# Kernel optimization log

Measured on AMD Instinct MI355X. Metric: run time of the kernel, lower is better.

## Reference

```python
import jax, jax.numpy as jnp
import numpy as np

N, E, D, H, G = 50000, 800000, 256, 256, 64
EPS = 1e-5

def setup_inputs() -> dict:
    key = jax.random.key(0)
    ks = jax.random.split(key, 16)
    s_in = float(np.sqrt(2.0 / D))   # He fan_in init
    s_h = float(np.sqrt(2.0 / H))
    inp = {}
    inp['x'] = jax.random.normal(ks[0], (N, D), jnp.float32)
    inp['edge_index'] = jax.random.randint(ks[1], (2, E), 0, N)
    inp['batch'] = jnp.sort(jax.random.randint(ks[2], (N,), 0, G))
    inp['bn_in_g'] = jnp.ones((D,), jnp.float32)
    inp['bn_in_b'] = jnp.zeros((D,), jnp.float32)
    for i in range(3):
        fan = D if i == 0 else H
        inp[f'W{i}'] = jax.random.normal(ks[3 + i], (fan, H), jnp.float32) * float(np.sqrt(2.0 / fan))
        inp[f'b{i}'] = jnp.zeros((H,), jnp.float32)
        inp[f'bn{i}_g'] = jnp.ones((H,), jnp.float32)
        inp[f'bn{i}_b'] = jnp.zeros((H,), jnp.float32)
    inp['Wa1'] = jax.random.normal(ks[6], (H, H // 2), jnp.float32) * s_h
    inp['ba1'] = jnp.zeros((H // 2,), jnp.float32)
    inp['Wa2'] = jax.random.normal(ks[7], (H // 2, 1), jnp.float32) * float(np.sqrt(2.0 / (H // 2)))
    inp['ba2'] = jnp.zeros((1,), jnp.float32)
    inp['Wo'] = jax.random.normal(ks[8], (H, 2), jnp.float32) * s_h
    inp['bo'] = jnp.zeros((2,), jnp.float32)
    return inp


def _bn(x, g, b):
    # BatchNorm1d, batch statistics (training-mode normalization), biased var
    m = jnp.mean(x, axis=0)
    v = jnp.mean(jnp.square(x - m), axis=0)
    return (x - m) * jax.lax.rsqrt(v + EPS) * g + b


def _gcn(x, src, dst, W, b):
    h = x @ W  # [N, H]
    n = x.shape[0]
    deg = jax.ops.segment_sum(jnp.ones_like(src, x.dtype), dst, num_segments=n) + 1.0  # +1 self-loop
    dinv = jax.lax.rsqrt(deg)  # [N]
    msg = h[src] * (dinv[src] * dinv[dst])[:, None]          # gather + edgewise scale
    agg = jax.ops.segment_sum(msg, dst, num_segments=n)      # scatter-add at dst
    return agg + h * (dinv * dinv)[:, None] + b               # self-loop term fused


def reference(x, edge_index, batch, bn_in_g, bn_in_b,
              W0, b0, bn0_g, bn0_b, W1, b1, bn1_g, bn1_b, W2, b2, bn2_g, bn2_b,
              Wa1, ba1, Wa2, ba2, Wo, bo):
    src, dst = edge_index[0], edge_index[1]
    x = _bn(x, bn_in_g, bn_in_b)  # dropout = identity (eval)
    # layer 0
    xp = _bn(jax.nn.relu(_gcn(x, src, dst, W0, b0)), bn0_g, bn0_b)
    # layers 1..2 with residual
    for (W, b, g, bb) in ((W1, b1, bn1_g, bn1_b), (W2, b2, bn2_g, bn2_b)):
        xn = _bn(jax.nn.relu(_gcn(xp, src, dst, W, b)), g, bb)
        xp = xn + xp
    # attention over all nodes (softmax along node dim, as in source)
    scores = jax.nn.leaky_relu(xp @ Wa1 + ba1, 0.01) @ Wa2 + ba2  # [N,1]
    w = jax.nn.softmax(scores, axis=0)
    xw = xp * w
    cnt = jax.ops.segment_sum(jnp.ones((xp.shape[0],), xp.dtype), batch, num_segments=G)
    pooled = jax.ops.segment_sum(xw, batch, num_segments=G) / jnp.maximum(cnt, 1.0)[:, None]
    return pooled @ Wo + bo  # [G, 2]
```

## Files before the change

### kernel.cpp

```cpp
#include <hip/hip_runtime.h>

#define N_NODES 50000
#define N_EDGES 800000
#define DIM 256
#define NG 64
#define EPS_BN 1e-5f
#define NB_AGG 3125
#define NB_COL 512
#define NSPLIT 32

typedef _Float16 f16;
typedef _Float16 half8 __attribute__((ext_vector_type(8)));
typedef _Float16 half4 __attribute__((ext_vector_type(4)));
typedef float floatx4 __attribute__((ext_vector_type(4)));

__device__ __forceinline__ int fkey(float f) { int i = __float_as_int(f); return (i >= 0) ? i : (i ^ 0x7fffffff); }
__device__ __forceinline__ float keyf(int k) { return __int_as_float((k >= 0) ? k : (k ^ 0x7fffffff)); }

__global__ __launch_bounds__(256) void col_stats_kernel(const float* __restrict__ X, int n,
                                                        float* __restrict__ part) {
    int c = threadIdx.x;
    float s = 0.f, q = 0.f;
    for (int i = blockIdx.x; i < n; i += gridDim.x) {
        float v = X[(size_t)i * DIM + c];
        s += v; q += v * v;
    }
    part[(size_t)blockIdx.x * 512 + c] = s;
    part[(size_t)blockIdx.x * 512 + DIM + c] = q;
}

__global__ __launch_bounds__(256) void reduce_finalize_kernel(const float* __restrict__ part, int nrows,
                                                              float* __restrict__ p2, int* __restrict__ counter,
                                                              const float* __restrict__ g, const float* __restrict__ b,
                                                              float* __restrict__ affine, float inv_n) {
    int col = blockIdx.x * 256 + threadIdx.x;
    int chunk = (nrows + NSPLIT - 1) / NSPLIT;
    int r0 = blockIdx.y * chunk;
    int r1 = min(r0 + chunk, nrows);
    float t = 0.f;
    for (int r = r0; r < r1; r++) t += part[(size_t)r * 512 + col];
    p2[(size_t)blockIdx.y * 512 + col] = t;
    __threadfence();
    __shared__ int lastf;
    if (threadIdx.x == 0) lastf = (atomicAdd(counter, 1) == 2 * NSPLIT - 1) ? 1 : 0;
    __syncthreads();
    if (lastf) {
        __threadfence();
        int c = threadIdx.x;
        float s = 0.f, q = 0.f;
#pragma unroll
        for (int r = 0; r < NSPLIT; r++) {
            s += p2[(size_t)r * 512 + c];
            q += p2[(size_t)r * 512 + DIM + c];
        }
        float m = s * inv_n;
        float v = q * inv_n - m * m;
        float rstd = rsqrtf(v + EPS_BN);
        float A = rstd * g[c];
        affine[c] = A;
        affine[DIM + c] = b[c] - m * A;
    }
}

__global__ void convert_all_kernel(const float* __restrict__ W0, const float* __restrict__ W1,
                                   const float* __restrict__ W2, const float* __restrict__ Wa1,
                                   f16* __restrict__ T0, f16* __restrict__ T1,
                                   f16* __restrict__ T2, f16* __restrict__ T3) {
    int idx = blockIdx.x * 256 + threadIdx.x;
    if (idx < 196608) {
        int w = idx >> 16, r = idx & 65535;
        const float* W = (w == 0) ? W0 : (w == 1) ? W1 : W2;
        f16* T = (w == 0) ? T0 : (w == 1) ? T1 : T2;
        int m = r >> 8, k = r & 255;
        T[r] = (f16)W[(size_t)k * 256 + m];
    } else {
        int r = idx - 196608;
        int m = r >> 8, k = r & 255;
        T3[r] = (f16)Wa1[(size_t)k * 128 + m];
    }
}

__global__ void count_bounds_kernel(const int* __restrict__ dst, int ne, int* __restrict__ cnt,
                                    const int* __restrict__ batch, int n, int* __restrict__ start) {
    int gb = blockIdx.x;
    if (gb < NB_AGG) {
        for (int i = gb * 256 + threadIdx.x; i < ne; i += NB_AGG * 256)
            atomicAdd(&cnt[dst[i]], 1);
    } else {
        int i = (gb - NB_AGG) * 256 + threadIdx.x;
        if (i < n) {
            int b = batch[i];
            if (i == 0 || batch[i - 1] != b) start[b] = i;
        }
    }
}

#define SCHUNK 2048
__global__ __launch_bounds__(256) void scan1_kernel(const int* __restrict__ cnt, int n,
                                                    int* __restrict__ outp, int* __restrict__ bsums,
                                                    float* __restrict__ dinv) {
    __shared__ int lds[256];
    int t = threadIdx.x;
    int base = blockIdx.x * SCHUNK + t * 8;
    int v[8]; int s = 0;
#pragma unroll
    for (int j = 0; j < 8; j++) {
        int id = base + j;
        int x = 0;
        if (id < n) { x = cnt[id]; dinv[id] = rsqrtf((float)x + 1.0f); }
        v[j] = s; s += x;
    }
    lds[t] = s; __syncthreads();
    for (int o = 1; o < 256; o <<= 1) {
        int add = (t >= o) ? lds[t - o] : 0;
        __syncthreads();
        lds[t] += add;
        __syncthreads();
    }
    int excl = lds[t] - s;
#pragma unroll
    for (int j = 0; j < 8; j++) { int id = base + j; if (id < n) outp[id] = excl + v[j]; }
    if (t == 255) bsums[blockIdx.x] = lds[255];
}

__global__ void scan3_kernel(int* __restrict__ outp, const int* __restrict__ bsums, int n, int total) {
    int i = blockIdx.x * blockDim.x + threadIdx.x;
    if (i < n) {
        int k = i / SCHUNK;
        int pref = 0;
        for (int j = 0; j < k; j++) pref += bsums[j];
        outp[i] += pref;
    }
    if (i == 0) outp[n] = total;
}

__global__ void scatter_kernel(const int* __restrict__ src, const int* __restrict__ dst, int ne,
                               const int* __restrict__ rowp, int* __restrict__ fill, int* __restrict__ ss) {
    for (int e = blockIdx.x * blockDim.x + threadIdx.x; e < ne; e += gridDim.x * blockDim.x) {
        int d = dst[e];
        int pos = rowp[d] + atomicAdd(&fill[d], 1);
        ss[pos] = src[e];
    }
}

__global__ void graph_offsets2_kernel(const int* __restrict__ start, int* __restrict__ off, int* __restrict__ cnt,
                                      int* __restrict__ maxkey) {
    if (threadIdx.x == 0 && blockIdx.x == 0) {
        int nxt = N_NODES;
        for (int g = NG - 1; g >= 0; --g) {
            int s = start[g];
            int o = (s < 0) ? nxt : s;
            off[g] = o;
            cnt[g] = nxt - o;
            nxt = o;
        }
        maxkey[0] = 0x80000000;
    }
}

__global__ __launch_bounds__(256) void gcn_agg_kernel(const f16* __restrict__ h, const int* __restrict__ rowp,
                                                      const int* __restrict__ ss, const float* __restrict__ dinv,
                                                      const float* __restrict__ bias, f16* __restrict__ out,
                                                      float* __restrict__ part, int n) {
    int wave = threadIdx.x >> 6;
    int lane = threadIdx.x & 63;
    int c = lane * 4;
    float4 bv = *(const float4*)&bias[c];
    float s0a = 0.f, s1a = 0.f, s2a = 0.f, s3a = 0.f;
    float q0a = 0.f, q1a = 0.f, q2a = 0.f, q3a = 0.f;
    for (int row = blockIdx.x * 4 + wave; row < n; row += gridDim.x * 4) {
        float ax = 0.f, ay = 0.f, az = 0.f, aw = 0.f;
        int e0 = rowp[row], e1 = rowp[row + 1];
        int e = e0;
        for (; e + 8 <= e1; e += 8) {
            int i0 = __builtin_amdgcn_readfirstlane(ss[e + 0]);
            int i1 = __builtin_amdgcn_readfirstlane(ss[e + 1]);
            int i2 = __builtin_amdgcn_readfirstlane(ss[e + 2]);
            int i3 = __builtin_amdgcn_readfirstlane(ss[e + 3]);
            int i4 = __builtin_amdgcn_readfirstlane(ss[e + 4]);
            int i5 = __builtin_amdgcn_readfirstlane(ss[e + 5]);
            int i6 = __builtin_amdgcn_readfirstlane(ss[e + 6]);
            int i7 = __builtin_amdgcn_readfirstlane(ss[e + 7]);
            half4 v0 = *(const half4*)&h[((size_t)i0 << 8) + c];
            half4 v1 = *(const half4*)&h[((size_t)i1 << 8) + c];
            half4 v2 = *(const half4*)&h[((size_t)i2 << 8) + c];
            half4 v3 = *(const half4*)&h[((size_t)i3 << 8) + c];
            half4 v4 = *(const half4*)&h[((size_t)i4 << 8) + c];
            half4 v5 = *(const half4*)&h[((size_t)i5 << 8) + c];
            half4 v6 = *(const half4*)&h[((size_t)i6 << 8) + c];
            half4 v7 = *(const half4*)&h[((size_t)i7 << 8) + c];
            ax += ((float)v0[0] + (float)v1[0]) + ((float)v2[0] + (float)v3[0]) +
                  ((float)v4[0] + (float)v5[0]) + ((float)v6[0] + (float)v7[0]);
            ay += ((float)v0[1] + (float)v1[1]) + ((float)v2[1] + (float)v3[1]) +
                  ((float)v4[1] + (float)v5[1]) + ((float)v6[1] + (float)v7[1]);
            az += ((float)v0[2] + (float)v1[2]) + ((float)v2[2] + (float)v3[2]) +
                  ((float)v4[2] + (float)v5[2]) + ((float)v6[2] + (float)v7[2]);
            aw += ((float)v0[3] + (float)v1[3]) + ((float)v2[3] + (float)v3[3]) +
                  ((float)v4[3] + (float)v5[3]) + ((float)v6[3] + (float)v7[3]);
        }
        for (; e < e1; e++) {
            int si = __builtin_amdgcn_readfirstlane(ss[e]);
            half4 hv = *(const half4*)&h[((size_t)si << 8) + c];
            ax += (float)hv[0]; ay += (float)hv[1]; az += (float)hv[2]; aw += (float)hv[3];
        }
        float di = dinv[row];
        half4 hs = *(const half4*)&h[((size_t)row << 8) + c];
        float rx = di * (ax + (float)hs[0]) + bv.x;
        float ry = di * (ay + (float)hs[1]) + bv.y;
        float rz = di * (az + (float)hs[2]) + bv.z;
        float rw = di * (aw + (float)hs[3]) + bv.w;
        half4 o; o[0] = (f16)rx; o[1] = (f16)ry; o[2] = (f16)rz; o[3] = (f16)rw;
        *(half4*)&out[((size_t)row << 8) + c] = o;
        float t;
        t = fmaxf(rx, 0.f); s0a += t; q0a += t * t;
        t = fmaxf(ry, 0.f); s1a += t; q1a += t * t;
        t = fmaxf(rz, 0.f); s2a += t; q2a += t * t;
        t = fmaxf(rw, 0.f); s3a += t; q3a += t * t;
    }
    __shared__ float sred[4][64][4];
    __shared__ float qred[4][64][4];
    sred[wave][lane][0] = s0a; sred[wave][lane][1] = s1a; sred[wave][lane][2] = s2a; sred[wave][lane][3] = s3a;
    qred[wave][lane][0] = q0a; qred[wave][lane][1] = q1a; qred[wave][lane][2] = q2a; qred[wave][lane][3] = q3a;
    __syncthreads();
    if (wave == 0) {
        size_t base = (size_t)blockIdx.x * 512;
        float4 a = make_float4(0.f, 0.f, 0.f, 0.f), qv = make_float4(0.f, 0.f, 0.f, 0.f);
#pragma unroll
        for (int ww = 0; ww < 4; ww++) {
            a.x += sred[ww][lane][0]; a.y += sred[ww][lane][1]; a.z += sred[ww][lane][2]; a.w += sred[ww][lane][3];
            qv.x += qred[ww][lane][0]; qv.y += qred[ww][lane][1]; qv.z += qred[ww][lane][2]; qv.w += qred[ww][lane][3];
        }
        *(float4*)&part[base + c] = a;
        *(float4*)&part[base + DIM + c] = qv;
    }
}

#define BM 128
#define BN 128
#define BK 32
#define LDP 40
__global__ __launch_bounds__(256) void gemm_fused_kernel(const float* __restrict__ Xf32, const f16* __restrict__ Ch,
                                                         const f16* __restrict__ Aold, f16* __restrict__ Afout,
                                                         const float* __restrict__ affine,
                                                         const f16* __restrict__ Wt, f16* __restrict__ Cout,
                                                         const float* __restrict__ scale, int n, int K, int M) {
    __shared__ __align__(16) f16 As[BM * LDP];
    __shared__ __align__(16) f16 Bs[BN * LDP];
    __shared__ float sA[256], sB[256];
    int tid = threadIdx.x;
    if (tid < 256) { sA[tid] = affine[tid]; sB[tid] = affine[256 + tid]; }
    int wave = tid >> 6, lane = tid & 63;
    int wm = wave >> 1, wn = wave & 1;
    int q = lane >> 4, l16 = lane & 15;
    int bm = blockIdx.x * BM, bn = blockIdx.y * BN;
    int kc = (tid & 3) * 8;
    int writer = (Afout != nullptr) && (blockIdx.y == 0);
    floatx4 acc[4][4] = {};
    __syncthreads();
    for (int k0 = 0; k0 < K; k0 += BK) {
        float a8[8], b8[8];
#pragma unroll
        for (int j = 0; j < 8; j++) { a8[j] = sA[k0 + kc + j]; b8[j] = sB[k0 + kc + j]; }
#pragma unroll
        for (int rr = 0; rr < 2; rr++) {
            int cidx = tid + rr * 256;
            int row = cidx >> 2;
            int arow = bm + row; if (arow >= n) arow = n - 1;
            float v[8];
            if (Xf32) {
                float4 x0 = *(const float4*)&Xf32[(size_t)arow * K + k0 + kc];
                float4 x1 = *(const float4*)&Xf32[(size_t)arow * K + k0 + kc + 4];
                v[0] = x0.x; v[1] = x0.y; v[2] = x0.z; v[3] = x0.w;
                v[4] = x1.x; v[5] = x1.y; v[6] = x1.z; v[7] = x1.w;
            } else {
                half8 ch = *(const half8*)&Ch[(size_t)arow * K + k0 + kc];
#pragma unroll
                for (int j = 0; j < 8; j++) v[j] = fmaxf((float)ch[j], 0.f);
            }
            half8 af;
            if (Aold) {
                half8 ao = *(const half8*)&Aold[(size_t)arow * K + k0 + kc];
#pragma unroll
                for (int j = 0; j < 8; j++) af[j] = (f16)(v[j] * a8[j] + b8[j] + (float)ao[j]);
            } else {
#pragma unroll
                for (int j = 0; j < 8; j++) af[j] = (f16)(v[j] * a8[j] + b8[j]);
            }
            *(float4*)&As[row * LDP + kc] = *(float4*)&af;
            if (writer && bm + row < n) *(half8*)&Afout[(size_t)arow * K + k0 + kc] = af;
            int brow = bn + row;
            *(float4*)&Bs[row * LDP + kc] = *(const float4*)&Wt[(size_t)brow * K + k0 + kc];
        }
        __syncthreads();
        half8 afr[4], bfr[4];
#pragma unroll
        for (int i = 0; i < 4; i++) afr[i] = *(half8*)&As[(wm * 64 + i * 16 + l16) * LDP + q * 8];
#pragma unroll
        for (int j = 0; j < 4; j++) bfr[j] = *(half8*)&Bs[(wn * 64 + j * 16 + l16) * LDP + q * 8];
#pragma unroll
        for (int i = 0; i < 4; i++)
#pragma unroll
            for (int j = 0; j < 4; j++)
                acc[i][j] = __builtin_amdgcn_mfma_f32_16x16x32_f16(afr[i], bfr[j], acc[i][j], 0, 0, 0);
        __syncthreads();
    }
#pragma unroll
    for (int i = 0; i < 4; i++) {
#pragma unroll
        for (int r = 0; r < 4; r++) {
            int row = bm + wm * 64 + i * 16 + q * 4 + r;
            if (row < n) {
                float sc = scale[row];
#pragma unroll
                for (int j = 0; j < 4; j++) {
                    int col = bn + wn * 64 + j * 16 + l16;
                    Cout[(size_t)row * M + col] = (f16)(acc[i][j][r] * sc);
                }
            }
        }
    }
}

__global__ __launch_bounds__(256) void gemm_attn_kernel(const f16* __restrict__ Ch, const f16* __restrict__ Aold,
                                                        f16* __restrict__ Afout, const float* __restrict__ affine,
                                                        const f16* __restrict__ Wt,
                                                        const float* __restrict__ ba1, const float* __restrict__ Wa2,
                                                        const float* __restrict__ ba2, float* __restrict__ score,
                                                        int* __restrict__ maxkey, int n, int K) {
    __shared__ __align__(16) f16 As[BM * LDP];
    __shared__ __align__(16) f16 Bs[128 * LDP];
    __shared__ float sA[256], sB[256];
    __shared__ float scred[128][2];
    int tid = threadIdx.x;
    if (tid < 256) { sA[tid] = affine[tid]; sB[tid] = affine[256 + tid]; }
    int wave = tid >> 6, lane = tid & 63;
    int wm = wave >> 1, wn = wave & 1;
    int q = lane >> 4, l16 = lane & 15;
    int bm = blockIdx.x * BM;
    int kc = (tid & 3) * 8;
    floatx4 acc[4][4] = {};
    __syncthreads();
    for (int k0 = 0; k0 < K; k0 += BK) {
        float a8[8], b8[8];
#pragma unroll
        for (int j = 0; j < 8; j++) { a8[j] = sA[k0 + kc + j]; b8[j] = sB[k0 + kc + j]; }
#pragma unroll
        for (int rr = 0; rr < 2; rr++) {
            int cidx = tid + rr * 256;
            int row = cidx >> 2;
            int arow = bm + row; if (arow >= n) arow = n - 1;
            half8 ch = *(const half8*)&Ch[(size_t)arow * K + k0 + kc];
            half8 ao = *(const half8*)&Aold[(size_t)arow * K + k0 + kc];
            half8 af;
#pragma unroll
            for (int j = 0; j < 8; j++)
                af[j] = (f16)(fmaxf((float)ch[j], 0.f) * a8[j] + b8[j] + (float)ao[j]);
            *(float4*)&As[row * LDP + kc] = *(float4*)&af;
            if (bm + row < n) *(half8*)&Afout[(size_t)arow * K + k0 + kc] = af;
            *(float4*)&Bs[row * LDP + kc] = *(const float4*)&Wt[(size_t)row * K + k0 + kc];
        }
        __syncthreads();
        half8 afr[4], bfr[4];
#pragma unroll
        for (int i = 0; i < 4; i++) afr[i] = *(half8*)&As[(wm * 64 + i * 16 + l16) * LDP + q * 8];
#pragma unroll
        for (int j = 0; j < 4; j++) bfr[j] = *(half8*)&Bs[(wn * 64 + j * 16 + l16) * LDP + q * 8];
#pragma unroll
        for (int i = 0; i < 4; i++)
#pragma unroll
            for (int j = 0; j < 4; j++)
                acc[i][j] = __builtin_amdgcn_mfma_f32_16x16x32_f16(afr[i], bfr[j], acc[i][j], 0, 0, 0);
        __syncthreads();
    }
    float ba1v[4], wa2v[4];
#pragma unroll
    for (int j = 0; j < 4; j++) {
        int col = wn * 64 + j * 16 + l16;
        ba1v[j] = ba1[col];
        wa2v[j] = Wa2[col];
    }
#pragma unroll
    for (int i = 0; i < 4; i++)
#pragma unroll
        for (int r = 0; r < 4; r++) {
            float p = 0.f;
#pragma unroll
            for (int j = 0; j < 4; j++) {
                float v = acc[i][j][r] + ba1v[j];
                v = (v > 0.f) ? v : 0.01f * v;
                p += v * wa2v[j];
            }
#pragma unroll
            for (int o = 1; o < 16; o <<= 1) p += __shfl_xor(p, o);
            if (l16 == 0) scred[wm * 64 + i * 16 + q * 4 + r][wn] = p;
        }
    __syncthreads();
    __shared__ float mred[128];
    if (tid < 128) {
        int grow = bm + tid;
        float sc = scred[tid][0] + scred[tid][1] + ba2[0];
        if (grow < n) score[grow] = sc; else sc = -3.0e38f;
        mred[tid] = sc;
    }
    __syncthreads();
    for (int o = 64; o > 0; o >>= 1) {
        if (tid < o && tid + o < 128) mred[tid] = fmaxf(mred[tid], mred[tid + o]);
        __syncthreads();
    }
    if (tid == 0) atomicMax(maxkey, fkey(mred[0]));
}

__global__ __launch_bounds__(256) void pool_kernel(const f16* __restrict__ Af, const float* __restrict__ score,
                                                   const int* __restrict__ offs, const int* __restrict__ cnts,
                                                   const int* __restrict__ maxkey, float* __restrict__ expsum,
                                                   float* __restrict__ pooled) {
    float mx = keyf(maxkey[0]);
    int c = threadIdx.x;
    int g = blockIdx.x;
    int st = offs[g], cn = cnts[g];
    float acc = 0.f, esum = 0.f;
    for (int i = (int)blockIdx.y; i < cn; i += 32) {
        int i1 = i + 8, i2 = i + 16, i3 = i + 24;
        float s0 = score[st + i];
        float s1 = (i1 < cn) ? score[st + i1] : -3.0e38f;
        float s2 = (i2 < cn) ? score[st + i2] : -3.0e38f;
        float s3 = (i3 < cn) ? score[st + i3] : -3.0e38f;
        float e0 = expf(s0 - mx), e1 = expf(s1 - mx), e2 = expf(s2 - mx), e3 = expf(s3 - mx);
        float a0 = (float)Af[(size_t)(st + i) * DIM + c];
        float a1 = (i1 < cn) ? (float)Af[(size_t)(st + i1) * DIM + c] : 0.f;
        float a2 = (i2 < cn) ? (float)Af[(size_t)(st + i2) * DIM + c] : 0.f;
        float a3 = (i3 < cn) ? (float)Af[(size_t)(st + i3) * DIM + c] : 0.f;
        acc += a0 * e0 + a1 * e1 + a2 * e2 + a3 * e3;
        esum += (e0 + e1) + (e2 + e3);
    }
    atomicAdd(&pooled[g * DIM + c], acc);
    if (c == 0) atomicAdd(expsum, esum);
}

__global__ __launch_bounds__(256) void out_kernel(const float* __restrict__ pooled, const int* __restrict__ cnt,
                                                  const float* __restrict__ expsum, const float* __restrict__ Wo,
                                                  const float* __restrict__ bo, float* __restrict__ out) {
    __shared__ float l0[256], l1[256];
    int g = blockIdx.x, c = threadIdx.x;
    float scale = 1.f / (expsum[0] * fmaxf((float)cnt[g], 1.f));
    float v = pooled[g * DIM + c] * scale;
    l0[c] = v * Wo[c * 2];
    l1[c] = v * Wo[c * 2 + 1];
    __syncthreads();
    for (int o = 128; o > 0; o >>= 1) {
        if (c < o) { l0[c] += l0[c + o]; l1[c] += l1[c + o]; }
        __syncthreads();
    }
    if (c == 0) { out[g * 2] = l0[0] + bo[0]; out[g * 2 + 1] = l1[0] + bo[1]; }
}

extern "C" void kernel_launch(void* const* d_in, const int* in_sizes, int n_in,
                              void* d_out, int out_size, void* d_ws, size_t ws_size,
                              hipStream_t stream) {
    const float* x       = (const float*)d_in[0];
    const int*   ei      = (const int*)d_in[1];
    const int*   batch   = (const int*)d_in[2];
    const float* bn_in_g = (const float*)d_in[3];
    const float* bn_in_b = (const float*)d_in[4];
    const float* Ws[3]   = {(const float*)d_in[5],  (const float*)d_in[9],  (const float*)d_in[13]};
    const float* bs[3]   = {(const float*)d_in[6],  (const float*)d_in[10], (const float*)d_in[14]};
    const float* gs[3]   = {(const float*)d_in[7],  (const float*)d_in[11], (const float*)d_in[15]};
    const float* bbs[3]  = {(const float*)d_in[8],  (const float*)d_in[12], (const float*)d_in[16]};
    const float* Wa1 = (const float*)d_in[17];
    const float* ba1 = (const float*)d_in[18];
    const float* Wa2 = (const float*)d_in[19];
    const float* ba2 = (const float*)d_in[20];
    const float* Wo  = (const float*)d_in[21];
    const float* bo  = (const float*)d_in[22];

    char* w = (char*)d_ws;
    size_t off = 0;
    auto alloc = [&](size_t bytes) -> void* {
        void* p = w + off;
        off += (bytes + 255) & ~(size_t)255;
        return p;
    };
    int*   deg     = (int*)alloc((size_t)N_NODES * 4);
    int*   fill    = (int*)alloc((size_t)N_NODES * 4);
    float* pooled  = (float*)alloc((size_t)NG * DIM * 4);
    int*   counters = (int*)alloc(4 * 4);
    float* expsum  = (float*)alloc(4);
    size_t zero_span = off;
    float* stats_part = (float*)alloc((size_t)NB_AGG * 512 * 4);
    float* stats_p2   = (float*)alloc((size_t)NSPLIT * 512 * 4);
    float* affine  = (float*)alloc(512 * 4);
    f16*   AfA  = (f16*)alloc((size_t)N_NODES * DIM * 2);
    f16*   AfB  = (f16*)alloc((size_t)N_NODES * DIM * 2);
    f16*   Bh   = (f16*)alloc((size_t)N_NODES * DIM * 2);
    f16*   Chb  = (f16*)alloc((size_t)N_NODES * DIM * 2);
    f16*   Wt[3];
    for (int l = 0; l < 3; l++) Wt[l] = (f16*)alloc((size_t)DIM * DIM * 2);
    f16*   Wa1t = (f16*)alloc((size_t)128 * DIM * 2);
    int* sorted_src = (int*)alloc((size_t)N_EDGES * 4);
    float* dinv = (float*)alloc((size_t)N_NODES * 4);
    int* rowp   = (int*)alloc((size_t)(N_NODES + 1) * 4);
    float* score = (float*)alloc((size_t)N_NODES * 4);
    int* bsums   = (int*)alloc(64 * 4);
    int* maxkey  = (int*)alloc(16);
    int* gstart  = (int*)alloc(64 * 4);
    int* cnt_g   = (int*)alloc(64 * 4);
    int* off_g   = (int*)alloc(64 * 4);

    const int* src = ei;
    const int* dst = ei + N_EDGES;
    const int NSCAN = (N_NODES + SCHUNK - 1) / SCHUNK;
    const float inv_n = 1.f / N_NODES;

    hipMemsetAsync(d_ws, 0, zero_span, stream);
    hipMemsetAsync(gstart, 0xff, 64 * 4, stream);

    count_bounds_kernel<<<NB_AGG + 196, 256, 0, stream>>>(dst, N_EDGES, deg, batch, N_NODES, gstart);
    scan1_kernel<<<NSCAN, 256, 0, stream>>>(deg, N_NODES, rowp, bsums, dinv);
    scan3_kernel<<<(N_NODES + 255) / 256, 256, 0, stream>>>(rowp, bsums, N_NODES, N_EDGES);
    scatter_kernel<<<NB_AGG, 256, 0, stream>>>(src, dst, N_EDGES, rowp, fill, sorted_src);
    graph_offsets2_kernel<<<1, 64, 0, stream>>>(gstart, off_g, cnt_g, maxkey);

    convert_all_kernel<<<896, 256, 0, stream>>>(Ws[0], Ws[1], Ws[2], Wa1, Wt[0], Wt[1], Wt[2], Wa1t);

    col_stats_kernel<<<NB_COL, 256, 0, stream>>>(x, N_NODES, stats_part);
    reduce_finalize_kernel<<<dim3(2, NSPLIT), 256, 0, stream>>>(stats_part, NB_COL, stats_p2, counters + 0,
                                                                bn_in_g, bn_in_b, affine, inv_n);

    dim3 ggrid((N_NODES + BM - 1) / BM, DIM / BN);
    gemm_fused_kernel<<<ggrid, 256, 0, stream>>>(x, nullptr, nullptr, nullptr, affine, Wt[0], Bh, dinv, N_NODES, DIM, DIM);
    gcn_agg_kernel<<<NB_AGG, 256, 0, stream>>>(Bh, rowp, sorted_src, dinv, bs[0], Chb, stats_part, N_NODES);
    reduce_finalize_kernel<<<dim3(2, NSPLIT), 256, 0, stream>>>(stats_part, NB_AGG, stats_p2, counters + 1,
                                                                gs[0], bbs[0], affine, inv_n);
    gemm_fused_kernel<<<ggrid, 256, 0, stream>>>(nullptr, Chb, nullptr, AfA, affine, Wt[1], Bh, dinv, N_NODES, DIM, DIM);
    gcn_agg_kernel<<<NB_AGG, 256, 0, stream>>>(Bh, rowp, sorted_src, dinv, bs[1], Chb, stats_part, N_NODES);
    reduce_finalize_kernel<<<dim3(2, NSPLIT), 256, 0, stream>>>(stats_part, NB_AGG, stats_p2, counters + 2,
                                                                gs[1], bbs[1], affine, inv_n);
    gemm_fused_kernel<<<ggrid, 256, 0, stream>>>(nullptr, Chb, AfA, AfB, affine, Wt[2], Bh, dinv, N_NODES, DIM, DIM);
    gcn_agg_kernel<<<NB_AGG, 256, 0, stream>>>(Bh, rowp, sorted_src, dinv, bs[2], Chb, stats_part, N_NODES);
    reduce_finalize_kernel<<<dim3(2, NSPLIT), 256, 0, stream>>>(stats_part, NB_AGG, stats_p2, counters + 3,
                                                                gs[2], bbs[2], affine, inv_n);

    gemm_attn_kernel<<<(N_NODES + BM - 1) / BM, 256, 0, stream>>>(Chb, AfB, AfA, affine, Wa1t,
                                                                  ba1, Wa2, ba2, score, maxkey, N_NODES, DIM);

    pool_kernel<<<dim3(NG, 8), 256, 0, stream>>>(AfA, score, off_g, cnt_g, maxkey, expsum, pooled);
    out_kernel<<<NG, 256, 0, stream>>>(pooled, cnt_g, expsum, Wo, bo, (float*)d_out);
}
```

Measured before the change: 743.4 us.

## Column-slice GCN aggregation across blocks and simplify stats reduction and CSR build

The aggregation kernel now splits the feature dimension into 8 column slices of 32, one slice per block. Each wave handles a row with 4 lane groups striding over edges, then reduces them with shuffles. The aim is to keep each slice's gather footprint small enough for cache reuse and to shrink the per-block partial stats. The two-level atomic-counter stats reduction is replaced by single-block finalize kernels. The CSR build records each edge's atomic position during counting, which removes the second atomic pass in scatter. In exchange, every edge index is read 8 times, and the gather width per lane drops to half2.

```diff
diff --git a/kernel.cpp b/kernel.cpp
--- a/kernel.cpp
+++ b/kernel.cpp
@@ -7,11 +7,12 @@
 #define EPS_BN 1e-5f
 #define NB_AGG 3125
 #define NB_COL 512
-#define NSPLIT 32
+#define NRG 391
 
 typedef _Float16 f16;
 typedef _Float16 half8 __attribute__((ext_vector_type(8)));
 typedef _Float16 half4 __attribute__((ext_vector_type(4)));
+typedef _Float16 half2 __attribute__((ext_vector_type(2)));
 typedef float floatx4 __attribute__((ext_vector_type(4)));
 
 __device__ __forceinline__ int fkey(float f) { int i = __float_as_int(f); return (i >= 0) ? i : (i ^ 0x7fffffff); }
@@ -29,37 +30,40 @@
     part[(size_t)blockIdx.x * 512 + DIM + c] = q;
 }
 
-__global__ __launch_bounds__(256) void reduce_finalize_kernel(const float* __restrict__ part, int nrows,
-                                                              float* __restrict__ p2, int* __restrict__ counter,
-                                                              const float* __restrict__ g, const float* __restrict__ b,
-                                                              float* __restrict__ affine, float inv_n) {
-    int col = blockIdx.x * 256 + threadIdx.x;
-    int chunk = (nrows + NSPLIT - 1) / NSPLIT;
-    int r0 = blockIdx.y * chunk;
-    int r1 = min(r0 + chunk, nrows);
-    float t = 0.f;
-    for (int r = r0; r < r1; r++) t += part[(size_t)r * 512 + col];
-    p2[(size_t)blockIdx.y * 512 + col] = t;
-    __threadfence();
-    __shared__ int lastf;
-    if (threadIdx.x == 0) lastf = (atomicAdd(counter, 1) == 2 * NSPLIT - 1) ? 1 : 0;
-    __syncthreads();
-    if (lastf) {
-        __threadfence();
-        int c = threadIdx.x;
-        float s = 0.f, q = 0.f;
-#pragma unroll
-        for (int r = 0; r < NSPLIT; r++) {
-            s += p2[(size_t)r * 512 + c];
-            q += p2[(size_t)r * 512 + DIM + c];
-        }
-        float m = s * inv_n;
-        float v = q * inv_n - m * m;
-        float rstd = rsqrtf(v + EPS_BN);
-        float A = rstd * g[c];
-        affine[c] = A;
-        affine[DIM + c] = b[c] - m * A;
-    }
+__global__ __launch_bounds__(256) void reduce_in_finalize_kernel(const float* __restrict__ part,
+                                                                 const float* __restrict__ g, const float* __restrict__ b,
+                                                                 float* __restrict__ affine, float inv_n) {
+    int c = threadIdx.x;
+    float s = 0.f, q = 0.f;
+    for (int r = 0; r < NB_COL; r++) {
+        s += part[(size_t)r * 512 + c];
+        q += part[(size_t)r * 512 + DIM + c];
+    }
+    float m = s * inv_n;
+    float v = q * inv_n - m * m;
+    float rstd = rsqrtf(v + EPS_BN);
+    float A = rstd * g[c];
+    affine[c] = A;
+    affine[DIM + c] = b[c] - m * A;
+}
+
+__global__ __launch_bounds__(256) void reduce_agg_finalize_kernel(const float* __restrict__ part,
+                                                                  const float* __restrict__ g, const float* __restrict__ b,
+                                                                  float* __restrict__ affine, float inv_n) {
+    int c = threadIdx.x;
+    int s_ = c >> 5, i32 = c & 31;
+    float s = 0.f, q = 0.f;
+    for (int rg = 0; rg < NRG; rg++) {
+        size_t base = (size_t)(rg * 8 + s_) * 64;
+        s += part[base + i32];
+        q += part[base + 32 + i32];
+    }
+    float m = s * inv_n;
+    float v = q * inv_n - m * m;
+    float rstd = rsqrtf(v + EPS_BN);
+    float A = rstd * g[c];
+    affine[c] = A;
+    affine[DIM + c] = b[c] - m * A;
 }
 
 __global__ void convert_all_kernel(const float* __restrict__ W0, const float* __restrict__ W1,
@@ -81,11 +85,12 @@
 }
 
 __global__ void count_bounds_kernel(const int* __restrict__ dst, int ne, int* __restrict__ cnt,
+                                    int* __restrict__ lpos,
                                     const int* __restrict__ batch, int n, int* __restrict__ start) {
     int gb = blockIdx.x;
     if (gb < NB_AGG) {
         for (int i = gb * 256 + threadIdx.x; i < ne; i += NB_AGG * 256)
-            atomicAdd(&cnt[dst[i]], 1);
+            lpos[i] = atomicAdd(&cnt[dst[i]], 1);
     } else {
         int i = (gb - NB_AGG) * 256 + threadIdx.x;
         if (i < n) {
@@ -134,13 +139,11 @@
     if (i == 0) outp[n] = total;
 }
 
-__global__ void scatter_kernel(const int* __restrict__ src, const int* __restrict__ dst, int ne,
-                               const int* __restrict__ rowp, int* __restrict__ fill, int* __restrict__ ss) {
-    for (int e = blockIdx.x * blockDim.x + threadIdx.x; e < ne; e += gridDim.x * blockDim.x) {
-        int d = dst[e];
-        int pos = rowp[d] + atomicAdd(&fill[d], 1);
-        ss[pos] = src[e];
-    }
+__global__ void scatter_kernel(const int* __restrict__ src, const int* __restrict__ dst,
+                               const int* __restrict__ lpos, int ne,
+                               const int* __restrict__ rowp, int* __restrict__ ss) {
+    for (int e = blockIdx.x * blockDim.x + threadIdx.x; e < ne; e += gridDim.x * blockDim.x)
+        ss[rowp[dst[e]] + lpos[e]] = src[e];
 }
 
 __global__ void graph_offsets2_kernel(const int* __restrict__ start, int* __restrict__ off, int* __restrict__ cnt,
@@ -162,76 +165,62 @@
                                                       const int* __restrict__ ss, const float* __restrict__ dinv,
                                                       const float* __restrict__ bias, f16* __restrict__ out,
                                                       float* __restrict__ part, int n) {
-    int wave = threadIdx.x >> 6;
-    int lane = threadIdx.x & 63;
-    int c = lane * 4;
-    float4 bv = *(const float4*)&bias[c];
-    float s0a = 0.f, s1a = 0.f, s2a = 0.f, s3a = 0.f;
-    float q0a = 0.f, q1a = 0.f, q2a = 0.f, q3a = 0.f;
-    for (int row = blockIdx.x * 4 + wave; row < n; row += gridDim.x * 4) {
-        float ax = 0.f, ay = 0.f, az = 0.f, aw = 0.f;
+    int blk = blockIdx.x;
+    int slice = blk & 7;
+    int rowgrp = blk >> 3;
+    int tid = threadIdx.x;
+    int wave = tid >> 6, lane = tid & 63;
+    int g = lane >> 4, t = lane & 15;
+    int colbase = slice * 32 + t * 2;
+    float b0 = bias[colbase], b1 = bias[colbase + 1];
+    float s0 = 0.f, s1 = 0.f, q0 = 0.f, q1 = 0.f;
+    for (int row = rowgrp * 4 + wave; row < n; row += NRG * 4) {
         int e0 = rowp[row], e1 = rowp[row + 1];
-        int e = e0;
-        for (; e + 8 <= e1; e += 8) {
-            int i0 = __builtin_amdgcn_readfirstlane(ss[e + 0]);
-            int i1 = __builtin_amdgcn_readfirstlane(ss[e + 1]);
-            int i2 = __builtin_amdgcn_readfirstlane(ss[e + 2]);
-            int i3 = __builtin_amdgcn_readfirstlane(ss[e + 3]);
-            int i4 = __builtin_amdgcn_readfirstlane(ss[e + 4]);
-            int i5 = __builtin_amdgcn_readfirstlane(ss[e + 5]);
-            int i6 = __builtin_amdgcn_readfirstlane(ss[e + 6]);
-            int i7 = __builtin_amdgcn_readfirstlane(ss[e + 7]);
-            half4 v0 = *(const half4*)&h[((size_t)i0 << 8) + c];
-            half4 v1 = *(const half4*)&h[((size_t)i1 << 8) + c];
-            half4 v2 = *(const half4*)&h[((size_t)i2 << 8) + c];
-            half4 v3 = *(const half4*)&h[((size_t)i3 << 8) + c];
-            half4 v4 = *(const half4*)&h[((size_t)i4 << 8) + c];
-            half4 v5 = *(const half4*)&h[((size_t)i5 << 8) + c];
-            half4 v6 = *(const half4*)&h[((size_t)i6 << 8) + c];
-            half4 v7 = *(const half4*)&h[((size_t)i7 << 8) + c];
-            ax += ((float)v0[0] + (float)v1[0]) + ((float)v2[0] + (float)v3[0]) +
-                  ((float)v4[0] + (float)v5[0]) + ((float)v6[0] + (float)v7[0]);
-            ay += ((float)v0[1] + (float)v1[1]) + ((float)v2[1] + (float)v3[1]) +
-                  ((float)v4[1] + (float)v5[1]) + ((float)v6[1] + (float)v7[1]);
-            az += ((float)v0[2] + (float)v1[2]) + ((float)v2[2] + (float)v3[2]) +
-                  ((float)v4[2] + (float)v5[2]) + ((float)v6[2] + (float)v7[2]);
-            aw += ((float)v0[3] + (float)v1[3]) + ((float)v2[3] + (float)v3[3]) +
-                  ((float)v4[3] + (float)v5[3]) + ((float)v6[3] + (float)v7[3]);
-        }
-        for (; e < e1; e++) {
-            int si = __builtin_amdgcn_readfirstlane(ss[e]);
-            half4 hv = *(const half4*)&h[((size_t)si << 8) + c];
-            ax += (float)hv[0]; ay += (float)hv[1]; az += (float)hv[2]; aw += (float)hv[3];
-        }
-        float di = dinv[row];
-        half4 hs = *(const half4*)&h[((size_t)row << 8) + c];
-        float rx = di * (ax + (float)hs[0]) + bv.x;
-        float ry = di * (ay + (float)hs[1]) + bv.y;
-        float rz = di * (az + (float)hs[2]) + bv.z;
-        float rw = di * (aw + (float)hs[3]) + bv.w;
-        half4 o; o[0] = (f16)rx; o[1] = (f16)ry; o[2] = (f16)rz; o[3] = (f16)rw;
-        *(half4*)&out[((size_t)row << 8) + c] = o;
-        float t;
-        t = fmaxf(rx, 0.f); s0a += t; q0a += t * t;
-        t = fmaxf(ry, 0.f); s1a += t; q1a += t * t;
-        t = fmaxf(rz, 0.f); s2a += t; q2a += t * t;
-        t = fmaxf(rw, 0.f); s3a += t; q3a += t * t;
-    }
-    __shared__ float sred[4][64][4];
-    __shared__ float qred[4][64][4];
-    sred[wave][lane][0] = s0a; sred[wave][lane][1] = s1a; sred[wave][lane][2] = s2a; sred[wave][lane][3] = s3a;
-    qred[wave][lane][0] = q0a; qred[wave][lane][1] = q1a; qred[wave][lane][2] = q2a; qred[wave][lane][3] = q3a;
+        float a0 = 0.f, a1 = 0.f;
+        int e = e0 + g;
+        for (; e + 4 < e1; e += 8) {
+            int sA = __builtin_nontemporal_load(&ss[e]);
+            int sB = __builtin_nontemporal_load(&ss[e + 4]);
+            half2 vA = *(const half2*)&h[((size_t)sA << 8) + colbase];
+            half2 vB = *(const half2*)&h[((size_t)sB << 8) + colbase];
+            a0 += (float)vA[0] + (float)vB[0];
+            a1 += (float)vA[1] + (float)vB[1];
+        }
+        if (e < e1) {
+            int sA = __builtin_nontemporal_load(&ss[e]);
+            half2 vA = *(const half2*)&h[((size_t)sA << 8) + colbase];
+            a0 += (float)vA[0];
+            a1 += (float)vA[1];
+        }
+        a0 += __shfl_xor(a0, 16); a0 += __shfl_xor(a0, 32);
+        a1 += __shfl_xor(a1, 16); a1 += __shfl_xor(a1, 32);
+        if (g == 0) {
+            float di = dinv[row];
+            half2 hs = *(const half2*)&h[((size_t)row << 8) + colbase];
+            float r0 = di * (a0 + (float)hs[0]) + b0;
+            float r1 = di * (a1 + (float)hs[1]) + b1;
+            half2 o; o[0] = (f16)r0; o[1] = (f16)r1;
+            *(half2*)&out[((size_t)row << 8) + colbase] = o;
+            float u;
+            u = fmaxf(r0, 0.f); s0 += u; q0 += u * u;
+            u = fmaxf(r1, 0.f); s1 += u; q1 += u * u;
+        }
+    }
+    __shared__ float sred[4][16][4];
+    if (g == 0) { sred[wave][t][0] = s0; sred[wave][t][1] = s1; sred[wave][t][2] = q0; sred[wave][t][3] = q1; }
     __syncthreads();
-    if (wave == 0) {
-        size_t base = (size_t)blockIdx.x * 512;
-        float4 a = make_float4(0.f, 0.f, 0.f, 0.f), qv = make_float4(0.f, 0.f, 0.f, 0.f);
-#pragma unroll
-        for (int ww = 0; ww < 4; ww++) {
-            a.x += sred[ww][lane][0]; a.y += sred[ww][lane][1]; a.z += sred[ww][lane][2]; a.w += sred[ww][lane][3];
-            qv.x += qred[ww][lane][0]; qv.y += qred[ww][lane][1]; qv.z += qred[ww][lane][2]; qv.w += qred[ww][lane][3];
-        }
-        *(float4*)&part[base + c] = a;
-        *(float4*)&part[base + DIM + c] = qv;
+    if (tid < 16) {
+        float S0 = 0.f, S1 = 0.f, Q0 = 0.f, Q1 = 0.f;
+#pragma unroll
+        for (int w2 = 0; w2 < 4; w2++) {
+            S0 += sred[w2][tid][0]; S1 += sred[w2][tid][1];
+            Q0 += sred[w2][tid][2]; Q1 += sred[w2][tid][3];
+        }
+        size_t base = (size_t)blk * 64;
+        part[base + tid * 2] = S0;
+        part[base + tid * 2 + 1] = S1;
+        part[base + 32 + tid * 2] = Q0;
+        part[base + 32 + tid * 2 + 1] = Q1;
     }
 }
 
@@ -481,13 +470,10 @@
         return p;
     };
     int*   deg     = (int*)alloc((size_t)N_NODES * 4);
-    int*   fill    = (int*)alloc((size_t)N_NODES * 4);
     float* pooled  = (float*)alloc((size_t)NG * DIM * 4);
-    int*   counters = (int*)alloc(4 * 4);
     float* expsum  = (float*)alloc(4);
     size_t zero_span = off;
-    float* stats_part = (float*)alloc((size_t)NB_AGG * 512 * 4);
-    float* stats_p2   = (float*)alloc((size_t)NSPLIT * 512 * 4);
+    float* stats_part = (float*)alloc((size_t)NB_COL * 512 * 4);
     float* affine  = (float*)alloc(512 * 4);
     f16*   AfA  = (f16*)alloc((size_t)N_NODES * DIM * 2);
     f16*   AfB  = (f16*)alloc((size_t)N_NODES * DIM * 2);
@@ -497,6 +483,7 @@
     for (int l = 0; l < 3; l++) Wt[l] = (f16*)alloc((size_t)DIM * DIM * 2);
     f16*   Wa1t = (f16*)alloc((size_t)128 * DIM * 2);
     int* sorted_src = (int*)alloc((size_t)N_EDGES * 4);
+    int* lpos   = (int*)alloc((size_t)N_EDGES * 4);
     float* dinv = (float*)alloc((size_t)N_NODES * 4);
     int* rowp   = (int*)alloc((size_t)(N_NODES + 1) * 4);
     float* score = (float*)alloc((size_t)N_NODES * 4);
@@ -514,31 +501,27 @@
     hipMemsetAsync(d_ws, 0, zero_span, stream);
     hipMemsetAsync(gstart, 0xff, 64 * 4, stream);
 
-    count_bounds_kernel<<<NB_AGG + 196, 256, 0, stream>>>(dst, N_EDGES, deg, batch, N_NODES, gstart);
+    count_bounds_kernel<<<NB_AGG + 196, 256, 0, stream>>>(dst, N_EDGES, deg, lpos, batch, N_NODES, gstart);
     scan1_kernel<<<NSCAN, 256, 0, stream>>>(deg, N_NODES, rowp, bsums, dinv);
     scan3_kernel<<<(N_NODES + 255) / 256, 256, 0, stream>>>(rowp, bsums, N_NODES, N_EDGES);
-    scatter_kernel<<<NB_AGG, 256, 0, stream>>>(src, dst, N_EDGES, rowp, fill, sorted_src);
+    scatter_kernel<<<NB_AGG, 256, 0, stream>>>(src, dst, lpos, N_EDGES, rowp, sorted_src);
     graph_offsets2_kernel<<<1, 64, 0, stream>>>(gstart, off_g, cnt_g, maxkey);
 
     convert_all_kernel<<<896, 256, 0, stream>>>(Ws[0], Ws[1], Ws[2], Wa1, Wt[0], Wt[1], Wt[2], Wa1t);
 
     col_stats_kernel<<<NB_COL, 256, 0, stream>>>(x, N_NODES, stats_part);
-    reduce_finalize_kernel<<<dim3(2, NSPLIT), 256, 0, stream>>>(stats_part, NB_COL, stats_p2, counters + 0,
-                                                                bn_in_g, bn_in_b, affine, inv_n);
+    reduce_in_finalize_kernel<<<1, 256, 0, stream>>>(stats_part, bn_in_g, bn_in_b, affine, inv_n);
 
     dim3 ggrid((N_NODES + BM - 1) / BM, DIM / BN);
     gemm_fused_kernel<<<ggrid, 256, 0, stream>>>(x, nullptr, nullptr, nullptr, affine, Wt[0], Bh, dinv, N_NODES, DIM, DIM);
-    gcn_agg_kernel<<<NB_AGG, 256, 0, stream>>>(Bh, rowp, sorted_src, dinv, bs[0], Chb, stats_part, N_NODES);
-    reduce_finalize_kernel<<<dim3(2, NSPLIT), 256, 0, stream>>>(stats_part, NB_AGG, stats_p2, counters + 1,
-                                                                gs[0], bbs[0], affine, inv_n);
+    gcn_agg_kernel<<<NRG * 8, 256, 0, stream>>>(Bh, rowp, sorted_src, dinv, bs[0], Chb, stats_part, N_NODES);
+    reduce_agg_finalize_kernel<<<1, 256, 0, stream>>>(stats_part, gs[0], bbs[0], affine, inv_n);
     gemm_fused_kernel<<<ggrid, 256, 0, stream>>>(nullptr, Chb, nullptr, AfA, affine, Wt[1], Bh, dinv, N_NODES, DIM, DIM);
-    gcn_agg_kernel<<<NB_AGG, 256, 0, stream>>>(Bh, rowp, sorted_src, dinv, bs[1], Chb, stats_part, N_NODES);
-    reduce_finalize_kernel<<<dim3(2, NSPLIT), 256, 0, stream>>>(stats_part, NB_AGG, stats_p2, counters + 2,
-                                                                gs[1], bbs[1], affine, inv_n);
+    gcn_agg_kernel<<<NRG * 8, 256, 0, stream>>>(Bh, rowp, sorted_src, dinv, bs[1], Chb, stats_part, N_NODES);
+    reduce_agg_finalize_kernel<<<1, 256, 0, stream>>>(stats_part, gs[1], bbs[1], affine, inv_n);
     gemm_fused_kernel<<<ggrid, 256, 0, stream>>>(nullptr, Chb, AfA, AfB, affine, Wt[2], Bh, dinv, N_NODES, DIM, DIM);
-    gcn_agg_kernel<<<NB_AGG, 256, 0, stream>>>(Bh, rowp, sorted_src, dinv, bs[2], Chb, stats_part, N_NODES);
-    reduce_finalize_kernel<<<dim3(2, NSPLIT), 256, 0, stream>>>(stats_part, NB_AGG, stats_p2, counters + 3,
-                                                                gs[2], bbs[2], affine, inv_n);
+    gcn_agg_kernel<<<NRG * 8, 256, 0, stream>>>(Bh, rowp, sorted_src, dinv, bs[2], Chb, stats_part, N_NODES);
+    reduce_agg_finalize_kernel<<<1, 256, 0, stream>>>(stats_part, gs[2], bbs[2], affine, inv_n);
 
     gemm_attn_kernel<<<(N_NODES + BM - 1) / BM, 256, 0, stream>>>(Chb, AfB, AfA, affine, Wa1t,
                                                                   ba1, Wa2, ba2, score, maxkey, N_NODES, DIM);
```

Measured after the change: 1.185 ms. +59.5%, slower.

## Reuse count-phase atomic slots for CSR scatter and shrink aggregation unroll

Applied to the files above, without the earlier changes.

The degree-count kernel now stores each edge's atomicAdd return value as its local slot. The scatter kernel then places source indices directly at rowp[dst]+slot, with no second round of atomics and no fill array. The GCN aggregation inner loop is cut from an 8-wide to a 4-wide unroll, and the readfirstlane calls on the neighbour indices are dropped. This saves the contended scatter atomics but adds an extra 3.2 MB buffer that is written once and read once, and it may reduce memory-level parallelism in the gather loop.

```diff
diff --git a/kernel.cpp b/kernel.cpp
--- a/kernel.cpp
+++ b/kernel.cpp
@@ -81,11 +81,12 @@
 }
 
 __global__ void count_bounds_kernel(const int* __restrict__ dst, int ne, int* __restrict__ cnt,
+                                    int* __restrict__ lpos,
                                     const int* __restrict__ batch, int n, int* __restrict__ start) {
     int gb = blockIdx.x;
     if (gb < NB_AGG) {
         for (int i = gb * 256 + threadIdx.x; i < ne; i += NB_AGG * 256)
-            atomicAdd(&cnt[dst[i]], 1);
+            lpos[i] = atomicAdd(&cnt[dst[i]], 1);
     } else {
         int i = (gb - NB_AGG) * 256 + threadIdx.x;
         if (i < n) {
@@ -134,13 +135,11 @@
     if (i == 0) outp[n] = total;
 }
 
-__global__ void scatter_kernel(const int* __restrict__ src, const int* __restrict__ dst, int ne,
-                               const int* __restrict__ rowp, int* __restrict__ fill, int* __restrict__ ss) {
-    for (int e = blockIdx.x * blockDim.x + threadIdx.x; e < ne; e += gridDim.x * blockDim.x) {
-        int d = dst[e];
-        int pos = rowp[d] + atomicAdd(&fill[d], 1);
-        ss[pos] = src[e];
-    }
+__global__ void scatter_kernel(const int* __restrict__ src, const int* __restrict__ dst,
+                               const int* __restrict__ lpos, int ne,
+                               const int* __restrict__ rowp, int* __restrict__ ss) {
+    for (int e = blockIdx.x * blockDim.x + threadIdx.x; e < ne; e += gridDim.x * blockDim.x)
+        ss[rowp[dst[e]] + lpos[e]] = src[e];
 }
 
 __global__ void graph_offsets2_kernel(const int* __restrict__ start, int* __restrict__ off, int* __restrict__ cnt,
@@ -172,34 +171,19 @@
         float ax = 0.f, ay = 0.f, az = 0.f, aw = 0.f;
         int e0 = rowp[row], e1 = rowp[row + 1];
         int e = e0;
-        for (; e + 8 <= e1; e += 8) {
-            int i0 = __builtin_amdgcn_readfirstlane(ss[e + 0]);
-            int i1 = __builtin_amdgcn_readfirstlane(ss[e + 1]);
-            int i2 = __builtin_amdgcn_readfirstlane(ss[e + 2]);
-            int i3 = __builtin_amdgcn_readfirstlane(ss[e + 3]);
-            int i4 = __builtin_amdgcn_readfirstlane(ss[e + 4]);
-            int i5 = __builtin_amdgcn_readfirstlane(ss[e + 5]);
-            int i6 = __builtin_amdgcn_readfirstlane(ss[e + 6]);
-            int i7 = __builtin_amdgcn_readfirstlane(ss[e + 7]);
-            half4 v0 = *(const half4*)&h[((size_t)i0 << 8) + c];
-            half4 v1 = *(const half4*)&h[((size_t)i1 << 8) + c];
-            half4 v2 = *(const half4*)&h[((size_t)i2 << 8) + c];
-            half4 v3 = *(const half4*)&h[((size_t)i3 << 8) + c];
-            half4 v4 = *(const half4*)&h[((size_t)i4 << 8) + c];
-            half4 v5 = *(const half4*)&h[((size_t)i5 << 8) + c];
-            half4 v6 = *(const half4*)&h[((size_t)i6 << 8) + c];
-            half4 v7 = *(const half4*)&h[((size_t)i7 << 8) + c];
-            ax += ((float)v0[0] + (float)v1[0]) + ((float)v2[0] + (float)v3[0]) +
-                  ((float)v4[0] + (float)v5[0]) + ((float)v6[0] + (float)v7[0]);
-            ay += ((float)v0[1] + (float)v1[1]) + ((float)v2[1] + (float)v3[1]) +
-                  ((float)v4[1] + (float)v5[1]) + ((float)v6[1] + (float)v7[1]);
-            az += ((float)v0[2] + (float)v1[2]) + ((float)v2[2] + (float)v3[2]) +
-                  ((float)v4[2] + (float)v5[2]) + ((float)v6[2] + (float)v7[2]);
-            aw += ((float)v0[3] + (float)v1[3]) + ((float)v2[3] + (float)v3[3]) +
-                  ((float)v4[3] + (float)v5[3]) + ((float)v6[3] + (float)v7[3]);
+        for (; e + 3 < e1; e += 4) {
+            int i0 = ss[e], i1 = ss[e + 1], i2 = ss[e + 2], i3 = ss[e + 3];
+            half4 h0 = *(const half4*)&h[((size_t)i0 << 8) + c];
+            half4 h1 = *(const half4*)&h[((size_t)i1 << 8) + c];
+            half4 h2 = *(const half4*)&h[((size_t)i2 << 8) + c];
+            half4 h3 = *(const half4*)&h[((size_t)i3 << 8) + c];
+            ax += ((float)h0[0] + (float)h1[0]) + ((float)h2[0] + (float)h3[0]);
+            ay += ((float)h0[1] + (float)h1[1]) + ((float)h2[1] + (float)h3[1]);
+            az += ((float)h0[2] + (float)h1[2]) + ((float)h2[2] + (float)h3[2]);
+            aw += ((float)h0[3] + (float)h1[3]) + ((float)h2[3] + (float)h3[3]);
         }
         for (; e < e1; e++) {
-            int si = __builtin_amdgcn_readfirstlane(ss[e]);
+            int si = ss[e];
             half4 hv = *(const half4*)&h[((size_t)si << 8) + c];
             ax += (float)hv[0]; ay += (float)hv[1]; az += (float)hv[2]; aw += (float)hv[3];
         }
@@ -481,7 +465,6 @@
         return p;
     };
     int*   deg     = (int*)alloc((size_t)N_NODES * 4);
-    int*   fill    = (int*)alloc((size_t)N_NODES * 4);
     float* pooled  = (float*)alloc((size_t)NG * DIM * 4);
     int*   counters = (int*)alloc(4 * 4);
     float* expsum  = (float*)alloc(4);
@@ -497,6 +480,7 @@
     for (int l = 0; l < 3; l++) Wt[l] = (f16*)alloc((size_t)DIM * DIM * 2);
     f16*   Wa1t = (f16*)alloc((size_t)128 * DIM * 2);
     int* sorted_src = (int*)alloc((size_t)N_EDGES * 4);
+    int* lpos   = (int*)alloc((size_t)N_EDGES * 4);
     float* dinv = (float*)alloc((size_t)N_NODES * 4);
     int* rowp   = (int*)alloc((size_t)(N_NODES + 1) * 4);
     float* score = (float*)alloc((size_t)N_NODES * 4);
@@ -514,10 +498,10 @@
     hipMemsetAsync(d_ws, 0, zero_span, stream);
     hipMemsetAsync(gstart, 0xff, 64 * 4, stream);
 
-    count_bounds_kernel<<<NB_AGG + 196, 256, 0, stream>>>(dst, N_EDGES, deg, batch, N_NODES, gstart);
+    count_bounds_kernel<<<NB_AGG + 196, 256, 0, stream>>>(dst, N_EDGES, deg, lpos, batch, N_NODES, gstart);
     scan1_kernel<<<NSCAN, 256, 0, stream>>>(deg, N_NODES, rowp, bsums, dinv);
     scan3_kernel<<<(N_NODES + 255) / 256, 256, 0, stream>>>(rowp, bsums, N_NODES, N_EDGES);
-    scatter_kernel<<<NB_AGG, 256, 0, stream>>>(src, dst, N_EDGES, rowp, fill, sorted_src);
+    scatter_kernel<<<NB_AGG, 256, 0, stream>>>(src, dst, lpos, N_EDGES, rowp, sorted_src);
     graph_offsets2_kernel<<<1, 64, 0, stream>>>(gstart, off_g, cnt_g, maxkey);
 
     convert_all_kernel<<<896, 256, 0, stream>>>(Ws[0], Ws[1], Ws[2], Wa1, Wt[0], Wt[1], Wt[2], Wa1t);
```

Measured after the change: 702.5 us. 5.5% less time.
